# Optimization experiments

Hardware: AMD Instinct MI355X
Metric: run time of the kernel (lower is better)

The kernel has to match this reference:

```python
import jax, jax.numpy as jnp
import numpy as np

B, T, C = 1, 2048, 1024
H = 16
D = C // H
FF = 4 * C


def layernorm(x, g, b, eps=1e-5):
    mu = jnp.mean(x, axis=-1, keepdims=True)
    var = jnp.var(x, axis=-1, keepdims=True)
    return (x - mu) * jax.lax.rsqrt(var + eps) * g + b


def setup_inputs() -> dict:
    key = jax.random.key(0)
    ks = jax.random.split(key, 16)
    s = 0.02
    return {
        "x": jax.random.normal(ks[0], (B, T, C), jnp.float32),
        "qkv_w": jax.random.normal(ks[1], (C, 3 * C), jnp.float32) * s,
        "qkv_b": jnp.zeros((3 * C,), jnp.float32),
        "out_w": jax.random.normal(ks[2], (C, C), jnp.float32) * s,
        "out_b": jnp.zeros((C,), jnp.float32),
        "ln1_g": jnp.ones((C,), jnp.float32),
        "ln1_b": jnp.zeros((C,), jnp.float32),
        "ln2_g": jnp.ones((C,), jnp.float32),
        "ln2_b": jnp.zeros((C,), jnp.float32),
        "w1": jax.random.normal(ks[3], (C, FF), jnp.float32) * s,
        "b1": jnp.zeros((FF,), jnp.float32),
        "w2": jax.random.normal(ks[4], (FF, C), jnp.float32) * s,
        "b2": jnp.zeros((C,), jnp.float32),
    }


def linear_attention(h, qkv_w, qkv_b, out_w, out_b):
    qkv = h @ qkv_w + qkv_b                      # (B,T,3C)
    q, k, v = jnp.split(qkv, 3, axis=-1)
    # (B,T,C) -> (B,H,T,D)
    reshape = lambda a: a.reshape(B, T, H, D).transpose(0, 2, 1, 3)
    q, k, v = reshape(q), reshape(k), reshape(v)
    Q = jax.nn.elu(q) + 1.0
    K = jax.nn.elu(k) + 1.0
    # causal linear attention via cumulative outer-products
    KV = jnp.einsum('bhtd,bhte->bhtde', K, v)    # (B,H,T,D,D)
    KV_cum = jnp.cumsum(KV, axis=2)
    K_cum = jnp.cumsum(K, axis=2)
    num = jnp.einsum('bhtd,bhtde->bhte', Q, KV_cum)
    den = jnp.einsum('bhtd,bhtd->bht', Q, K_cum)[..., None]
    o = num / (den + 1e-6)                       # (B,H,T,D)
    o = o.transpose(0, 2, 1, 3).reshape(B, T, C)
    return o @ out_w + out_b


def reference(x, qkv_w, qkv_b, out_w, out_b, ln1_g, ln1_b, ln2_g, ln2_b, w1, b1, w2, b2):
    x = x + linear_attention(layernorm(x, ln1_g, ln1_b), qkv_w, qkv_b, out_w, out_b)
    h = layernorm(x, ln2_g, ln2_b)
    mlp = jax.nn.gelu(h @ w1 + b1, approximate=False) @ w2 + b2
    return x + mlp
```

## Files before the change

kernel.cpp:

```cpp
#include <hip/hip_runtime.h>

typedef unsigned short u16;
typedef __bf16 bf16x8 __attribute__((ext_vector_type(8)));
typedef float f32x4 __attribute__((ext_vector_type(4)));
typedef unsigned short u16x8 __attribute__((ext_vector_type(8)));
typedef unsigned short u16x4 __attribute__((ext_vector_type(4)));

__device__ __forceinline__ float bf2f(u16 u){
  union { unsigned i; float f; } v; v.i = ((unsigned)u) << 16; return v.f;
}
__device__ __forceinline__ u16 f2bf(float f){
  union { float f; unsigned i; } v; v.f = f;
  unsigned r = v.i + 0x7FFFu + ((v.i >> 16) & 1u);
  return (u16)(r >> 16);
}
__device__ __forceinline__ float elup(float x){ return x > 0.f ? x + 1.f : expf(x); }

__device__ __forceinline__ void gload_lds16(const void* gsrc, void* ldst){
  __builtin_amdgcn_global_load_lds(
      (__attribute__((address_space(1))) void*)(unsigned long long)gsrc,
      (__attribute__((address_space(3))) void*)(unsigned)(unsigned long long)ldst,
      16, 0, 0);
}

struct TD { const float* in; u16* out; int R, Cc, cx, ntiles; };

__global__ __launch_bounds__(256) void transpose4(TD d0, TD d1, TD d2, TD d3){
  __shared__ u16 tile[32][33];
  int b = blockIdx.x;
  TD d;
  if (b < d0.ntiles) d = d0;
  else { b -= d0.ntiles;
    if (b < d1.ntiles) d = d1;
    else { b -= d1.ntiles;
      if (b < d2.ntiles) d = d2;
      else { b -= d2.ntiles; d = d3; } } }
  int c0 = (b % d.cx) * 32, r0 = (b / d.cx) * 32;
  int tx = threadIdx.x, ty = threadIdx.y;
  #pragma unroll
  for (int i=0;i<4;i++)
    tile[ty + i*8][tx] = f2bf(d.in[(size_t)(r0 + ty + i*8)*d.Cc + c0 + tx]);
  __syncthreads();
  #pragma unroll
  for (int i=0;i<4;i++)
    d.out[(size_t)(c0 + ty + i*8)*d.R + r0 + tx] = tile[tx][ty + i*8];
}

__global__ __launch_bounds__(256) void ln_f32(const float* __restrict__ x, const float* __restrict__ g,
                                              const float* __restrict__ b, u16* __restrict__ y){
  int row = blockIdx.x, tid = threadIdx.x;
  size_t base = (size_t)row*1024 + tid*4;
  f32x4 xv = *(const f32x4*)(x + base);
  float v0=xv[0], v1=xv[1], v2=xv[2], v3=xv[3];
  float s  = v0+v1+v2+v3;
  float s2 = v0*v0+v1*v1+v2*v2+v3*v3;
  #pragma unroll
  for (int off=32; off>0; off>>=1){ s += __shfl_xor(s, off); s2 += __shfl_xor(s2, off); }
  __shared__ float ls[4], ls2[4];
  if ((tid & 63) == 0){ ls[tid>>6] = s; ls2[tid>>6] = s2; }
  __syncthreads();
  float ts = ls[0]+ls[1]+ls[2]+ls[3];
  float ts2 = ls2[0]+ls2[1]+ls2[2]+ls2[3];
  float mean = ts*(1.f/1024.f);
  float var  = ts2*(1.f/1024.f) - mean*mean;
  float rstd = rsqrtf(var + 1e-5f);
  f32x4 gv = *(const f32x4*)(g + tid*4);
  f32x4 bv = *(const f32x4*)(b + tid*4);
  u16x4 ov;
  ov[0]=f2bf((v0-mean)*rstd*gv[0]+bv[0]);
  ov[1]=f2bf((v1-mean)*rstd*gv[1]+bv[1]);
  ov[2]=f2bf((v2-mean)*rstd*gv[2]+bv[2]);
  ov[3]=f2bf((v3-mean)*rstd*gv[3]+bv[3]);
  *(u16x4*)(y + base) = ov;
}

__global__ __launch_bounds__(256) void ln2_fused(const u16* __restrict__ P0, const u16* __restrict__ P1,
                                                 const u16* __restrict__ P2, const u16* __restrict__ P3,
                                                 const float* __restrict__ bias, const float* __restrict__ xres,
                                                 const float* __restrict__ g, const float* __restrict__ b,
                                                 float* __restrict__ x2, u16* __restrict__ h2){
  int row = blockIdx.x, tid = threadIdx.x;
  size_t base = (size_t)row*1024 + tid*4;
  u16x4 a0 = *(const u16x4*)(P0 + base);
  u16x4 a1 = *(const u16x4*)(P1 + base);
  u16x4 a2 = *(const u16x4*)(P2 + base);
  u16x4 a3 = *(const u16x4*)(P3 + base);
  f32x4 rv = *(const f32x4*)(xres + base);
  f32x4 bv = *(const f32x4*)(bias + tid*4);
  f32x4 v;
  #pragma unroll
  for (int j=0;j<4;j++) v[j] = (bf2f(a0[j])+bf2f(a1[j])) + (bf2f(a2[j])+bf2f(a3[j])) + bv[j] + rv[j];
  *(f32x4*)(x2 + base) = v;
  float s  = v[0]+v[1]+v[2]+v[3];
  float s2 = v[0]*v[0]+v[1]*v[1]+v[2]*v[2]+v[3]*v[3];
  #pragma unroll
  for (int off=32; off>0; off>>=1){ s += __shfl_xor(s, off); s2 += __shfl_xor(s2, off); }
  __shared__ float ls[4], ls2[4];
  if ((tid & 63) == 0){ ls[tid>>6] = s; ls2[tid>>6] = s2; }
  __syncthreads();
  float ts = ls[0]+ls[1]+ls[2]+ls[3];
  float ts2 = ls2[0]+ls2[1]+ls2[2]+ls2[3];
  float mean = ts*(1.f/1024.f);
  float var  = ts2*(1.f/1024.f) - mean*mean;
  float rstd = rsqrtf(var + 1e-5f);
  f32x4 gv = *(const f32x4*)(g + tid*4);
  f32x4 bb = *(const f32x4*)(b + tid*4);
  u16x4 ov;
  #pragma unroll
  for (int j=0;j<4;j++) ov[j] = f2bf((v[j]-mean)*rstd*gv[j]+bb[j]);
  *(u16x4*)(h2 + base) = ov;
}

template<int EPI>
__global__ __launch_bounds__(512) void gemm_bt(const u16* __restrict__ A, const u16* __restrict__ BT,
                                               const float* __restrict__ bias, const float* __restrict__ res,
                                               void* __restrict__ out, int N, int K, size_t pstride){
  __shared__ u16 As[2][128*32];
  __shared__ u16 Bs[2][128*32];
  int tid = threadIdx.x;
  int w = tid >> 6, lane = tid & 63;
  int m0 = blockIdx.x * 128, n0 = blockIdx.y * 128;
  int Kc = K / gridDim.z;
  int kbase = blockIdx.z * Kc;
  int nt = Kc / 32;

  f32x4 acc[2][4] = {};

  const u16* aSrc = A  + (size_t)(m0 + w*16 + (lane>>2))*K + kbase + (lane&3)*8;
  const u16* bSrc = BT + (size_t)(n0 + w*16 + (lane>>2))*K + kbase + (lane&3)*8;
  int r0 = (w>>1)*32, c0 = (w&1)*64;
  int lrow = lane & 15, lk = (lane>>4)*8;

  {
    gload_lds16(aSrc, As[0] + w*512);
    gload_lds16(bSrc, Bs[0] + w*512);
  }
  __syncthreads();

  int cur = 0;
  for (int t = 0; t < nt; ++t){
    if (t + 1 < nt){
      int k0 = (t+1)*32;
      gload_lds16(aSrc + k0, As[cur^1] + w*512);
      gload_lds16(bSrc + k0, Bs[cur^1] + w*512);
    }
    const u16* Ab = As[cur];
    const u16* Bb = Bs[cur];
    bf16x8 af[2], bfv[4];
    #pragma unroll
    for (int mi=0;mi<2;mi++) af[mi]  = *(const bf16x8*)(Ab + (r0 + mi*16 + lrow)*32 + lk);
    #pragma unroll
    for (int ni=0;ni<4;ni++) bfv[ni] = *(const bf16x8*)(Bb + (c0 + ni*16 + lrow)*32 + lk);
    #pragma unroll
    for (int mi=0;mi<2;mi++)
      #pragma unroll
      for (int ni=0;ni<4;ni++)
        acc[mi][ni] = __builtin_amdgcn_mfma_f32_16x16x32_bf16(af[mi], bfv[ni], acc[mi][ni], 0, 0, 0);
    __syncthreads();
    cur ^= 1;
  }

  int lgr = lane >> 4;
  u16* pout = (EPI == 3) ? ((u16*)out + (size_t)blockIdx.z * pstride) : (u16*)out;
  #pragma unroll
  for (int mi=0;mi<2;mi++){
    #pragma unroll
    for (int j=0;j<4;j++){
      int row = m0 + r0 + mi*16 + lgr*4 + j;
      #pragma unroll
      for (int ni=0;ni<4;ni++){
        int col = n0 + c0 + ni*16 + lrow;
        size_t idx = (size_t)row*N + col;
        if constexpr (EPI == 3){
          pout[idx] = f2bf(acc[mi][ni][j]);
        } else {
          float v = acc[mi][ni][j] + bias[col];
          if constexpr (EPI == 0){
            ((u16*)out)[idx] = f2bf(v);
          } else {
            v = 0.5f * v * (1.f + erff(v * 0.70710678118654752f));
            ((u16*)out)[idx] = f2bf(v);
          }
        }
      }
    }
  }
}

__global__ __launch_bounds__(256) void reduce4(const u16* __restrict__ P0, const u16* __restrict__ P1,
                                               const u16* __restrict__ P2, const u16* __restrict__ P3,
                                               const float* __restrict__ bias, const float* __restrict__ res,
                                               float* __restrict__ out){
  size_t i = ((size_t)blockIdx.x*256 + threadIdx.x)*4;
  u16x4 a = *(const u16x4*)(P0 + i);
  u16x4 b = *(const u16x4*)(P1 + i);
  u16x4 c = *(const u16x4*)(P2 + i);
  u16x4 d = *(const u16x4*)(P3 + i);
  f32x4 rv = *(const f32x4*)(res + i);
  f32x4 bv = *(const f32x4*)(bias + (i & 1023));
  f32x4 o;
  #pragma unroll
  for (int j=0;j<4;j++) o[j] = (bf2f(a[j]) + bf2f(b[j])) + (bf2f(c[j]) + bf2f(d[j])) + bv[j] + rv[j];
  *(f32x4*)(out + i) = o;
}

__global__ __launch_bounds__(256) void attn_chunksum(const u16* __restrict__ qkv, float* __restrict__ S,
                                                     float* __restrict__ Ks){
  __shared__ u16 KT[64*72];
  __shared__ u16 VT[64*72];
  int c = blockIdx.x, h = blockIdx.y, tid = threadIdx.x;
  int t = tid >> 2, seg = tid & 3, e0 = seg*16;
  size_t rowb = (size_t)(c*64 + t)*3072 + h*64 + e0;
  u16x8 k0 = *(const u16x8*)(qkv + rowb + 1024);
  u16x8 k1 = *(const u16x8*)(qkv + rowb + 1032);
  u16x8 v0 = *(const u16x8*)(qkv + rowb + 2048);
  u16x8 v1 = *(const u16x8*)(qkv + rowb + 2056);
  #pragma unroll
  for (int i=0;i<8;i++){
    KT[(e0 + i)*72 + t]     = f2bf(elup(bf2f(k0[i])));
    KT[(e0 + 8 + i)*72 + t] = f2bf(elup(bf2f(k1[i])));
    VT[(e0 + i)*72 + t]     = v0[i];
    VT[(e0 + 8 + i)*72 + t] = v1[i];
  }
  __syncthreads();

  int w = tid >> 6, lane = tid & 63;
  int lr = lane & 15, lk = (lane>>4)*8, g = lane >> 4, cl = lane & 15;
  bf16x8 av_[2];
  #pragma unroll
  for (int kk=0;kk<2;kk++) av_[kk] = *(const bf16x8*)(VT + (w*16 + lr)*72 + kk*32 + lk);
  f32x4 acc[4] = {};
  #pragma unroll
  for (int di=0;di<4;di++){
    #pragma unroll
    for (int kk=0;kk<2;kk++){
      bf16x8 bk = *(const bf16x8*)(KT + (di*16 + lr)*72 + kk*32 + lk);
      acc[di] = __builtin_amdgcn_mfma_f32_16x16x32_bf16(av_[kk], bk, acc[di], 0, 0, 0);
    }
  }
  size_t base = (size_t)(h*32 + c)*4096;
  #pragma unroll
  for (int di=0;di<4;di++)
    #pragma unroll
    for (int j=0;j<4;j++)
      S[base + (size_t)(w*16 + g*4 + j)*64 + di*16 + cl] = acc[di][j];

  float s = 0.f;
  #pragma unroll
  for (int i=0;i<16;i++) s += bf2f(KT[t*72 + e0 + i]);
  s += __shfl_xor(s, 1); s += __shfl_xor(s, 2);
  if (seg == 0) Ks[(size_t)(h*32 + c)*64 + t] = s;
}

__global__ __launch_bounds__(256) void attn_prefix(float* __restrict__ S, float* __restrict__ Ks){
  int g = blockIdx.x, h = blockIdx.y, tid = threadIdx.x;
  size_t hb = (size_t)h * 32 * 4096;
  int idx = g*256 + tid;
  float run = 0.f;
  for (int c=0; c<32; c++){
    size_t p = hb + (size_t)c*4096 + idx;
    float v = S[p]; S[p] = run; run += v;
  }
  if (g == 0 && tid < 64){
    float r2 = 0.f;
    for (int c=0; c<32; c++){
      size_t p = (size_t)(h*32 + c)*64 + tid;
      float v = Ks[p]; Ks[p] = r2; r2 += v;
    }
  }
}

__global__ __launch_bounds__(256) void attn_out(const u16* __restrict__ qkv, const float* __restrict__ S,
                                                const float* __restrict__ Ks, u16* __restrict__ o){
  __shared__ u16 Qs [64*72];
  __shared__ u16 Ksh[64*72];
  __shared__ u16 VT [64*72];
  __shared__ u16 SpT[64*72];
  __shared__ u16 Am [64*72];
  __shared__ float kp[64], den[64];
  int c = blockIdx.x, h = blockIdx.y, tid = threadIdx.x;
  int t = tid >> 2, seg = tid & 3, e0 = seg*16;

  size_t rowb = (size_t)(c*64 + t)*3072 + h*64 + e0;
  u16x8 q0 = *(const u16x8*)(qkv + rowb);
  u16x8 q1 = *(const u16x8*)(qkv + rowb + 8);
  u16x8 k0 = *(const u16x8*)(qkv + rowb + 1024);
  u16x8 k1 = *(const u16x8*)(qkv + rowb + 1032);
  u16x8 v0 = *(const u16x8*)(qkv + rowb + 2048);
  u16x8 v1 = *(const u16x8*)(qkv + rowb + 2056);
  #pragma unroll
  for (int i=0;i<8;i++){
    Qs [t*72 + e0 + i]     = f2bf(elup(bf2f(q0[i])));
    Qs [t*72 + e0 + 8 + i] = f2bf(elup(bf2f(q1[i])));
    Ksh[t*72 + e0 + i]     = f2bf(elup(bf2f(k0[i])));
    Ksh[t*72 + e0 + 8 + i] = f2bf(elup(bf2f(k1[i])));
    VT [(e0 + i)*72 + t]     = v0[i];
    VT [(e0 + 8 + i)*72 + t] = v1[i];
  }
  size_t sbase = (size_t)(h*32 + c)*4096;
  {
    const f32x4* sp = (const f32x4*)(S + sbase + (size_t)t*64 + e0);
    #pragma unroll
    for (int qd=0;qd<4;qd++){
      f32x4 v = sp[qd];
      #pragma unroll
      for (int j=0;j<4;j++) SpT[t*72 + e0 + qd*4 + j] = f2bf(v[j]);
    }
  }
  if (tid < 64) kp[tid] = Ks[(size_t)(h*32 + c)*64 + tid];
  __syncthreads();

  int w = tid >> 6, lane = tid & 63;
  int lr = lane & 15, lk = (lane>>4)*8, g = lane >> 4, cl = lane & 15;

  bf16x8 aq[2];
  #pragma unroll
  for (int kk=0;kk<2;kk++) aq[kk] = *(const bf16x8*)(Qs + (w*16 + lr)*72 + kk*32 + lk);

  f32x4 acc[4] = {};
  #pragma unroll
  for (int ni=0;ni<4;ni++){
    #pragma unroll
    for (int kk=0;kk<2;kk++){
      bf16x8 bs = *(const bf16x8*)(SpT + (ni*16 + lr)*72 + kk*32 + lk);
      acc[ni] = __builtin_amdgcn_mfma_f32_16x16x32_bf16(aq[kk], bs, acc[ni], 0, 0, 0);
    }
  }
  #pragma unroll
  for (int si=0;si<4;si++){
    f32x4 qk = {};
    #pragma unroll
    for (int kk=0;kk<2;kk++){
      bf16x8 bk = *(const bf16x8*)(Ksh + (si*16 + lr)*72 + kk*32 + lk);
      qk = __builtin_amdgcn_mfma_f32_16x16x32_bf16(aq[kk], bk, qk, 0, 0, 0);
    }
    #pragma unroll
    for (int j=0;j<4;j++){
      int rowt = w*16 + g*4 + j;
      int scol = si*16 + cl;
      Am[rowt*72 + scol] = f2bf((scol <= rowt) ? qk[j] : 0.f);
    }
  }
  __syncthreads();

  {
    float dsum = 0.f;
    #pragma unroll
    for (int i=0;i<16;i++) dsum += bf2f(Am[t*72 + e0 + i]);
    #pragma unroll
    for (int i=0;i<16;i++) dsum += bf2f(Qs[t*72 + e0 + i]) * kp[e0 + i];
    dsum += __shfl_xor(dsum, 1); dsum += __shfl_xor(dsum, 2);
    if (seg == 0) den[t] = dsum;
  }
  {
    bf16x8 aa[2];
    #pragma unroll
    for (int kk=0;kk<2;kk++) aa[kk] = *(const bf16x8*)(Am + (w*16 + lr)*72 + kk*32 + lk);
    #pragma unroll
    for (int ni=0;ni<4;ni++){
      #pragma unroll
      for (int kk=0;kk<2;kk++){
        bf16x8 bv = *(const bf16x8*)(VT + (ni*16 + lr)*72 + kk*32 + lk);
        acc[ni] = __builtin_amdgcn_mfma_f32_16x16x32_bf16(aa[kk], bv, acc[ni], 0, 0, 0);
      }
    }
  }
  __syncthreads();

  #pragma unroll
  for (int j=0;j<4;j++){
    int rowt = w*16 + g*4 + j;
    float inv = 1.f/(den[rowt] + 1e-6f);
    #pragma unroll
    for (int ni=0;ni<4;ni++)
      o[(size_t)(c*64 + rowt)*1024 + h*64 + ni*16 + cl] = f2bf(acc[ni][j]*inv);
  }
}

extern "C" void kernel_launch(void* const* d_in, const int* in_sizes, int n_in,
                              void* d_out, int out_size, void* d_ws, size_t ws_size,
                              hipStream_t stream) {
  (void)in_sizes; (void)n_in; (void)out_size; (void)ws_size;
  const float* x     = (const float*)d_in[0];
  const float* qkv_w = (const float*)d_in[1];
  const float* qkv_b = (const float*)d_in[2];
  const float* out_w = (const float*)d_in[3];
  const float* out_b = (const float*)d_in[4];
  const float* ln1_g = (const float*)d_in[5];
  const float* ln1_b = (const float*)d_in[6];
  const float* ln2_g = (const float*)d_in[7];
  const float* ln2_b = (const float*)d_in[8];
  const float* w1    = (const float*)d_in[9];
  const float* b1    = (const float*)d_in[10];
  const float* w2    = (const float*)d_in[11];
  const float* b2    = (const float*)d_in[12];

  char* ws = (char*)d_ws;
  u16*   wT_qkv = (u16*)  (ws);
  u16*   wT_out = (u16*)  (ws +  6291456);
  u16*   wT_w1  = (u16*)  (ws +  8388608);
  u16*   wT_w2  = (u16*)  (ws + 16777216);
  u16*   h1     = (u16*)  (ws + 25165824);
  u16*   qkv    = (u16*)  (ws + 29360128);
  float* Ssum   = (float*)(ws + 41943040);
  float* ksum   = (float*)(ws + 50331648);
  float* x2     = (float*)(ws + 50462720);
  u16*   h2     = (u16*)  (ws + 58851328);
  u16*   o      = h1;
  u16*   a1     = qkv;
  u16*   Pa0    = (u16*)(ws + 29360128);
  size_t PaStride = 2097152;
  u16*   Pm0    = (u16*)(ws);
  u16*   Pm1    = (u16*)(ws +  4194304);
  u16*   Pm2    = (u16*)(ws +  8388608);
  u16*   Pm3    = (u16*)(ws + 12582912);
  size_t PmStride = 2097152;
  float* outp   = (float*)d_out;

  TD t0{qkv_w, wT_qkv, 1024, 3072,  96, 3072};
  TD t1{out_w, wT_out, 1024, 1024,  32, 1024};
  TD t2{w1,    wT_w1,  1024, 4096, 128, 4096};
  TD t3{w2,    wT_w2,  4096, 1024,  32, 4096};
  transpose4<<<12288, dim3(32,8), 0, stream>>>(t0, t1, t2, t3);

  ln_f32<<<2048, 256, 0, stream>>>(x, ln1_g, ln1_b, h1);
  gemm_bt<0><<<dim3(16, 24, 1), 512, 0, stream>>>(h1, wT_qkv, qkv_b, nullptr, qkv, 3072, 1024, 0);

  attn_chunksum<<<dim3(32, 16), 256, 0, stream>>>(qkv, Ssum, ksum);
  attn_prefix  <<<dim3(16, 16), 256, 0, stream>>>(Ssum, ksum);
  attn_out     <<<dim3(32, 16), 256, 0, stream>>>(qkv, Ssum, ksum, o);

  gemm_bt<3><<<dim3(16, 8, 4), 512, 0, stream>>>(o, wT_out, nullptr, nullptr, Pa0, 1024, 1024, PaStride);
  ln2_fused<<<2048, 256, 0, stream>>>(Pa0, Pa0 + PaStride, Pa0 + 2*PaStride, Pa0 + 3*PaStride,
                                      out_b, x, ln2_g, ln2_b, x2, h2);

  gemm_bt<1><<<dim3(16, 32, 1), 512, 0, stream>>>(h2, wT_w1, b1, nullptr, a1, 4096, 1024, 0);

  gemm_bt<3><<<dim3(16, 8, 4), 512, 0, stream>>>(a1, wT_w2, nullptr, nullptr, Pm0, 1024, 4096, PmStride);
  reduce4<<<2048, 256, 0, stream>>>(Pm0, Pm1, Pm2, Pm3, b2, x2, outp);
}
```

Measured before the change: 142.7 us.

## Double GEMM K-tile with XOR-swizzled LDS and merge LN1 into transpose kernel

The GEMM K-step grows from 32 to 64, so each stage loads twice as much data per barrier, and an XOR swizzle on the LDS layout avoids bank conflicts on the wider rows. Occupancy is hinted with launch_bounds(512,4). Separately, the layernorm-1 kernel is folded into the weight-transpose launch as extra blocks, removing one launch. In exchange, LDS use doubles to 64 KB per block, which may lower occupancy.

Measured after the change: 129.4 us. 9.3% less time.

```diff
diff --git a/kernel.cpp b/kernel.cpp
--- a/kernel.cpp
+++ b/kernel.cpp
@@ -25,18 +25,48 @@
 
 struct TD { const float* in; u16* out; int R, Cc, cx, ntiles; };
 
-__global__ __launch_bounds__(256) void transpose4(TD d0, TD d1, TD d2, TD d3){
+__global__ __launch_bounds__(256) void prep(TD d0, TD d1, TD d2, TD d3,
+                                            const float* __restrict__ x, const float* __restrict__ g,
+                                            const float* __restrict__ b, u16* __restrict__ y){
   __shared__ u16 tile[32][33];
-  int b = blockIdx.x;
+  __shared__ float ls[4], ls2[4];
+  int bidx = blockIdx.x, tid = threadIdx.x;
+  if (bidx >= 12288){
+    int row = bidx - 12288;
+    size_t base = (size_t)row*1024 + tid*4;
+    f32x4 xv = *(const f32x4*)(x + base);
+    float v0=xv[0], v1=xv[1], v2=xv[2], v3=xv[3];
+    float s  = v0+v1+v2+v3;
+    float s2 = v0*v0+v1*v1+v2*v2+v3*v3;
+    #pragma unroll
+    for (int off=32; off>0; off>>=1){ s += __shfl_xor(s, off); s2 += __shfl_xor(s2, off); }
+    if ((tid & 63) == 0){ ls[tid>>6] = s; ls2[tid>>6] = s2; }
+    __syncthreads();
+    float ts = ls[0]+ls[1]+ls[2]+ls[3];
+    float ts2 = ls2[0]+ls2[1]+ls2[2]+ls2[3];
+    float mean = ts*(1.f/1024.f);
+    float var  = ts2*(1.f/1024.f) - mean*mean;
+    float rstd = rsqrtf(var + 1e-5f);
+    f32x4 gv = *(const f32x4*)(g + tid*4);
+    f32x4 bv = *(const f32x4*)(b + tid*4);
+    u16x4 ov;
+    ov[0]=f2bf((v0-mean)*rstd*gv[0]+bv[0]);
+    ov[1]=f2bf((v1-mean)*rstd*gv[1]+bv[1]);
+    ov[2]=f2bf((v2-mean)*rstd*gv[2]+bv[2]);
+    ov[3]=f2bf((v3-mean)*rstd*gv[3]+bv[3]);
+    *(u16x4*)(y + base) = ov;
+    return;
+  }
+  int bb = bidx;
   TD d;
-  if (b < d0.ntiles) d = d0;
-  else { b -= d0.ntiles;
-    if (b < d1.ntiles) d = d1;
-    else { b -= d1.ntiles;
-      if (b < d2.ntiles) d = d2;
-      else { b -= d2.ntiles; d = d3; } } }
-  int c0 = (b % d.cx) * 32, r0 = (b / d.cx) * 32;
-  int tx = threadIdx.x, ty = threadIdx.y;
+  if (bb < d0.ntiles) d = d0;
+  else { bb -= d0.ntiles;
+    if (bb < d1.ntiles) d = d1;
+    else { bb -= d1.ntiles;
+      if (bb < d2.ntiles) d = d2;
+      else { bb -= d2.ntiles; d = d3; } } }
+  int c0 = (bb % d.cx) * 32, r0 = (bb / d.cx) * 32;
+  int tx = tid & 31, ty = tid >> 5;
   #pragma unroll
   for (int i=0;i<4;i++)
     tile[ty + i*8][tx] = f2bf(d.in[(size_t)(r0 + ty + i*8)*d.Cc + c0 + tx]);
@@ -44,34 +74,6 @@
   #pragma unroll
   for (int i=0;i<4;i++)
     d.out[(size_t)(c0 + ty + i*8)*d.R + r0 + tx] = tile[tx][ty + i*8];
-}
-
-__global__ __launch_bounds__(256) void ln_f32(const float* __restrict__ x, const float* __restrict__ g,
-                                              const float* __restrict__ b, u16* __restrict__ y){
-  int row = blockIdx.x, tid = threadIdx.x;
-  size_t base = (size_t)row*1024 + tid*4;
-  f32x4 xv = *(const f32x4*)(x + base);
-  float v0=xv[0], v1=xv[1], v2=xv[2], v3=xv[3];
-  float s  = v0+v1+v2+v3;
-  float s2 = v0*v0+v1*v1+v2*v2+v3*v3;
-  #pragma unroll
-  for (int off=32; off>0; off>>=1){ s += __shfl_xor(s, off); s2 += __shfl_xor(s2, off); }
-  __shared__ float ls[4], ls2[4];
-  if ((tid & 63) == 0){ ls[tid>>6] = s; ls2[tid>>6] = s2; }
-  __syncthreads();
-  float ts = ls[0]+ls[1]+ls[2]+ls[3];
-  float ts2 = ls2[0]+ls2[1]+ls2[2]+ls2[3];
-  float mean = ts*(1.f/1024.f);
-  float var  = ts2*(1.f/1024.f) - mean*mean;
-  float rstd = rsqrtf(var + 1e-5f);
-  f32x4 gv = *(const f32x4*)(g + tid*4);
-  f32x4 bv = *(const f32x4*)(b + tid*4);
-  u16x4 ov;
-  ov[0]=f2bf((v0-mean)*rstd*gv[0]+bv[0]);
-  ov[1]=f2bf((v1-mean)*rstd*gv[1]+bv[1]);
-  ov[2]=f2bf((v2-mean)*rstd*gv[2]+bv[2]);
-  ov[3]=f2bf((v3-mean)*rstd*gv[3]+bv[3]);
-  *(u16x4*)(y + base) = ov;
 }
 
 __global__ __launch_bounds__(256) void ln2_fused(const u16* __restrict__ P0, const u16* __restrict__ P1,
@@ -112,50 +114,64 @@
 }
 
 template<int EPI>
-__global__ __launch_bounds__(512) void gemm_bt(const u16* __restrict__ A, const u16* __restrict__ BT,
-                                               const float* __restrict__ bias, const float* __restrict__ res,
-                                               void* __restrict__ out, int N, int K, size_t pstride){
-  __shared__ u16 As[2][128*32];
-  __shared__ u16 Bs[2][128*32];
+__global__ __launch_bounds__(512, 4) void gemm_bt(const u16* __restrict__ A, const u16* __restrict__ BT,
+                                                  const float* __restrict__ bias, const float* __restrict__ res,
+                                                  void* __restrict__ out, int N, int K, size_t pstride){
+  __shared__ u16 As[2][128*64];
+  __shared__ u16 Bs[2][128*64];
   int tid = threadIdx.x;
   int w = tid >> 6, lane = tid & 63;
   int m0 = blockIdx.x * 128, n0 = blockIdx.y * 128;
   int Kc = K / gridDim.z;
   int kbase = blockIdx.z * Kc;
-  int nt = Kc / 32;
+  int nt = Kc / 64;
 
   f32x4 acc[2][4] = {};
 
-  const u16* aSrc = A  + (size_t)(m0 + w*16 + (lane>>2))*K + kbase + (lane&3)*8;
-  const u16* bSrc = BT + (size_t)(n0 + w*16 + (lane>>2))*K + kbase + (lane&3)*8;
+  int l3 = lane >> 3, l7 = lane & 7;
+  const u16* aSrc = A  + (size_t)(m0 + w*16 + l3)*K + kbase + (l7 ^ l3)*8;
+  const u16* bSrc = BT + (size_t)(n0 + w*16 + l3)*K + kbase + (l7 ^ l3)*8;
   int r0 = (w>>1)*32, c0 = (w&1)*64;
-  int lrow = lane & 15, lk = (lane>>4)*8;
+  int lrow = lane & 15, g4 = lane >> 4;
+  int swz = (lrow & 7) << 4;
 
   {
-    gload_lds16(aSrc, As[0] + w*512);
-    gload_lds16(bSrc, Bs[0] + w*512);
+    u16* aD = As[0] + w*16*64;
+    u16* bD = Bs[0] + w*16*64;
+    gload_lds16(aSrc,                aD);
+    gload_lds16(aSrc + (size_t)8*K,  aD + 8*64);
+    gload_lds16(bSrc,                bD);
+    gload_lds16(bSrc + (size_t)8*K,  bD + 8*64);
   }
   __syncthreads();
 
   int cur = 0;
   for (int t = 0; t < nt; ++t){
     if (t + 1 < nt){
-      int k0 = (t+1)*32;
-      gload_lds16(aSrc + k0, As[cur^1] + w*512);
-      gload_lds16(bSrc + k0, Bs[cur^1] + w*512);
-    }
-    const u16* Ab = As[cur];
-    const u16* Bb = Bs[cur];
-    bf16x8 af[2], bfv[4];
-    #pragma unroll
-    for (int mi=0;mi<2;mi++) af[mi]  = *(const bf16x8*)(Ab + (r0 + mi*16 + lrow)*32 + lk);
-    #pragma unroll
-    for (int ni=0;ni<4;ni++) bfv[ni] = *(const bf16x8*)(Bb + (c0 + ni*16 + lrow)*32 + lk);
-    #pragma unroll
-    for (int mi=0;mi<2;mi++)
-      #pragma unroll
-      for (int ni=0;ni<4;ni++)
-        acc[mi][ni] = __builtin_amdgcn_mfma_f32_16x16x32_bf16(af[mi], bfv[ni], acc[mi][ni], 0, 0, 0);
+      int k0 = (t+1)*64;
+      u16* aD = As[cur^1] + w*16*64;
+      u16* bD = Bs[cur^1] + w*16*64;
+      gload_lds16(aSrc + k0,               aD);
+      gload_lds16(aSrc + (size_t)8*K + k0, aD + 8*64);
+      gload_lds16(bSrc + k0,               bD);
+      gload_lds16(bSrc + (size_t)8*K + k0, bD + 8*64);
+    }
+    const char* Ab = (const char*)As[cur];
+    const char* Bb = (const char*)Bs[cur];
+    #pragma unroll
+    for (int kk=0; kk<2; kk++){
+      int ko = (kk*64 + g4*16) ^ swz;
+      bf16x8 af[2], bfv[4];
+      #pragma unroll
+      for (int mi=0;mi<2;mi++) af[mi]  = *(const bf16x8*)(Ab + (r0 + mi*16 + lrow)*128 + ko);
+      #pragma unroll
+      for (int ni=0;ni<4;ni++) bfv[ni] = *(const bf16x8*)(Bb + (c0 + ni*16 + lrow)*128 + ko);
+      #pragma unroll
+      for (int mi=0;mi<2;mi++)
+        #pragma unroll
+        for (int ni=0;ni<4;ni++)
+          acc[mi][ni] = __builtin_amdgcn_mfma_f32_16x16x32_bf16(af[mi], bfv[ni], acc[mi][ni], 0, 0, 0);
+    }
     __syncthreads();
     cur ^= 1;
   }
@@ -421,9 +437,8 @@
   TD t1{out_w, wT_out, 1024, 1024,  32, 1024};
   TD t2{w1,    wT_w1,  1024, 4096, 128, 4096};
   TD t3{w2,    wT_w2,  4096, 1024,  32, 4096};
-  transpose4<<<12288, dim3(32,8), 0, stream>>>(t0, t1, t2, t3);
-
-  ln_f32<<<2048, 256, 0, stream>>>(x, ln1_g, ln1_b, h1);
+  prep<<<14336, 256, 0, stream>>>(t0, t1, t2, t3, x, ln1_g, ln1_b, h1);
+
   gemm_bt<0><<<dim3(16, 24, 1), 512, 0, stream>>>(h1, wT_qkv, qkv_b, nullptr, qkv, 3072, 1024, 0);
 
   attn_chunksum<<<dim3(32, 16), 256, 0, stream>>>(qkv, Ssum, ksum);
```
